# Performance work log

Measured on AMD Instinct MI355X. Metric: run time of the kernel, lower is better.

The kernel has to match this reference:

```python
import jax, jax.numpy as jnp
import numpy as np

B, D = 8192, 256
NUM_CLASSES = 128
CHUNK = 256          # matches module chunk_size; B % CHUNK == 0
TEMP = 0.07
EPS_NORM = 1e-12


def setup_inputs() -> dict:
    key = jax.random.key(0)
    k1, k2 = jax.random.split(key)
    features = jax.random.normal(k1, (B, D), dtype=jnp.float32)
    labels = jax.random.randint(k2, (B,), 0, NUM_CLASSES, dtype=jnp.int64)
    return {"features": features, "labels": labels}


def reference(features, labels):
    n = features.shape[0]
    temperature = max(TEMP, 1e-4)

    # F.normalize(dim=1): x / max(||x||, eps)
    norm = jnp.maximum(jnp.linalg.norm(features, axis=1, keepdims=True), EPS_NORM)
    f = features / norm
    # clamp is a no-op after normalization but kept for faithfulness
    f = jnp.clip(f, -1000.0, 1000.0)

    # [B, B] similarity; the torch loop computes exactly these rows chunk by chunk
    sim = jnp.matmul(f, f.T) / temperature

    # self-mask: each row i masks column i (diagonal of its chunk's square block)
    self_mask = ~jnp.eye(n, dtype=bool)

    # positive mask: same label, excluding self
    pos = (labels[:, None] == labels[None, :]) & self_mask
    # per-chunk fallback: if a 256-row chunk has no positives at all, use self_mask
    pos_c = pos.reshape(n // CHUNK, CHUNK, n)
    has_pos = pos_c.any(axis=(1, 2), keepdims=True)
    pos = jnp.where(has_pos, pos_c, self_mask.reshape(n // CHUNK, CHUNK, n)).reshape(n, n)

    # max-subtract BEFORE self-masking (faithful: includes self-sim = 1/temp)
    sim_max = jnp.max(sim, axis=1, keepdims=True)
    logits = jnp.clip(sim - jax.lax.stop_gradient(sim_max), -1000.0, 1000.0)

    exp_sim = jnp.maximum(jnp.exp(logits), 1e-8) * self_mask
    log_sum_exp = jnp.log(jnp.sum(exp_sim, axis=1, keepdims=True) + 1e-8)
    log_prob = jnp.maximum(logits - log_sum_exp, -1000.0)

    pos_pairs = jnp.sum(pos, axis=1)                      # [B] int
    row_loss = -jnp.sum(pos * log_prob, axis=1)           # [B]
    valid = pos_pairs > 0
    row_loss = jnp.where(valid, row_loss / jnp.maximum(pos_pairs, 1).astype(row_loss.dtype), 0.0)

    total_loss = jnp.sum(row_loss)
    total_pairs = jnp.sum(valid).astype(jnp.float32)
    mean_loss = total_loss / (total_pairs + 1e-8)
    loss = mean_loss  # reduction == 'mean'
    return loss, total_pairs, mean_loss
```

## Files before the change

kernel.cpp:

```cpp
#include <hip/hip_runtime.h>
#include <hip/hip_bf16.h>
#include <type_traits>

#define NB 8192
#define DD 256
#define INV_T (1.0f/0.07f)
#define LOG2E 1.4426950408889634f
#define K1    (INV_T*LOG2E)
#define CEXP  6.2087204553847255e-7f
#define NSTRIP 32
#define TILE 256
#define BN 64
#define NITER 4
#define BUFB (BN*DD*2)

typedef __attribute__((ext_vector_type(8))) short s8v;
typedef __attribute__((ext_vector_type(4))) float f4v;
typedef unsigned int u32;
typedef unsigned short u16;

#define OFF_FB   0
#define OFF_SE   (4*1024*1024)
#define OFF_SP   (OFF_SE + NSTRIP*NB*4)
#define OFF_CL   (OFF_SP + NSTRIP*NB*4)
#define OFF_CV   (OFF_CL + 256)
#define OFF_CNT  (OFF_CV + 256)

__global__ void k_norm(const float* __restrict__ feat,
                       __hip_bfloat16* __restrict__ fb, int* __restrict__ cnt) {
    if (blockIdx.x == 0 && threadIdx.x == 0) *cnt = 0;
    const int t = threadIdx.x;
    const int w = t >> 6, l = t & 63;
    const int row = blockIdx.x * 4 + w;
    const float4 v = ((const float4*)feat)[row * 64 + l];
    float s = v.x * v.x + v.y * v.y + v.z * v.z + v.w * v.w;
    #pragma unroll
    for (int d = 32; d; d >>= 1) s += __shfl_xor(s, d, 64);
    const float scale = 1.0f / fmaxf(sqrtf(s), 1e-12f);
    __hip_bfloat16 h0 = __float2bfloat16(v.x * scale);
    __hip_bfloat16 h1 = __float2bfloat16(v.y * scale);
    __hip_bfloat16 h2 = __float2bfloat16(v.z * scale);
    __hip_bfloat16 h3 = __float2bfloat16(v.w * scale);
    ushort4 o;
    o.x = *(u16*)&h0; o.y = *(u16*)&h1; o.z = *(u16*)&h2; o.w = *(u16*)&h3;
    ((ushort4*)fb)[row * 64 + l] = o;
}

__launch_bounds__(512)
__global__ void k_main(const __hip_bfloat16* __restrict__ fb,
                       const int* __restrict__ lab,
                       float* __restrict__ SE, float* __restrict__ SP) {
    __shared__ __align__(16) char ldsB[2 * BUFB];
    __shared__ int ldsLab[TILE];
    __shared__ float ldsColE[8][TILE];
    __shared__ float ldsColP[8][TILE];
    const int tid = threadIdx.x;
    const int w = tid >> 6;
    const int l = tid & 63;
    const int l15 = l & 15, lg = l >> 4;

    int cb = 0, rem = blockIdx.x;
    while (rem >= NSTRIP - cb) { rem -= NSTRIP - cb; cb++; }
    const int rb = cb + rem;
    const int row0 = rb * TILE, col0 = cb * TILE;
    const int wbase = row0 + w * 32;

    if (tid < TILE) ldsLab[tid] = lab[col0 + tid];

    s8v a[2][8];
    #pragma unroll
    for (int m = 0; m < 2; m++)
        #pragma unroll
        for (int kk = 0; kk < 8; kk++)
            a[m][kk] = *(const s8v*)(fb + (wbase + m * 16 + l15) * DD + kk * 32 + lg * 8);

    int labr[8];
    #pragma unroll
    for (int m = 0; m < 2; m++)
        #pragma unroll
        for (int r = 0; r < 4; r++)
            labr[m * 4 + r] = lab[wbase + m * 16 + lg * 4 + r];

    float sE[8], sPa[8], colE[4], colP[4];
    #pragma unroll
    for (int i = 0; i < 8; i++) { sE[i] = 0.f; sPa[i] = 0.f; }
    #pragma unroll
    for (int i = 0; i < 4; i++) { colE[i] = 0.f; colP[i] = 0.f; }

    s8v st[4];
    auto load_tile = [&](int ct) {
        const char* gsrc = (const char*)fb + (size_t)(col0 + ct * BN) * (DD * 2);
        #pragma unroll
        for (int i = 0; i < 4; i++)
            st[i] = *(const s8v*)(gsrc + tid * 16 + i * 8192);
    };
    auto write_tile = [&](int bufoff) {
        #pragma unroll
        for (int i = 0; i < 4; i++) {
            const int x = tid * 16 + i * 8192;
            const int br = x >> 9, inrow = x & 511;
            *(s8v*)(ldsB + bufoff + (br * 512 | (inrow ^ ((br & 7) << 4)))) = st[i];
        }
    };

    auto run = [&](auto diagC) {
        constexpr bool DIAG = decltype(diagC)::value;
        load_tile(0);
        write_tile(0);
        __syncthreads();
        for (int ct = 0; ct < NITER; ct++) {
            const int curoff = (ct & 1) * BUFB;
            if (ct + 1 < NITER) load_tile(ct + 1);

            int lc[4];
            #pragma unroll
            for (int n = 0; n < 4; n++)
                lc[n] = ldsLab[ct * BN + n * 16 + l15];

            f4v acc[2][4];
            #pragma unroll
            for (int m = 0; m < 2; m++)
                #pragma unroll
                for (int n = 0; n < 4; n++)
                    acc[m][n] = (f4v){0.f, 0.f, 0.f, 0.f};

            #pragma unroll
            for (int kk = 0; kk < 8; kk++) {
                s8v bfr[4];
                #pragma unroll
                for (int n = 0; n < 4; n++) {
                    const int br = n * 16 + l15;
                    const int ad = (br * 512 + kk * 64 + lg * 16) ^ ((br & 7) << 4);
                    bfr[n] = *(const s8v*)(ldsB + curoff + ad);
                }
                #pragma unroll
                for (int m = 0; m < 2; m++)
                    #pragma unroll
                    for (int n = 0; n < 4; n++)
                        acc[m][n] = __builtin_amdgcn_mfma_f32_16x16x32_bf16(a[m][kk], bfr[n], acc[m][n], 0, 0, 0);
            }

            #pragma unroll
            for (int n = 0; n < 4; n++) {
                #pragma unroll
                for (int m = 0; m < 2; m++)
                    #pragma unroll
                    for (int r = 0; r < 4; r++) {
                        const int idx = m * 4 + r;
                        const float v = acc[m][n][r];
                        float e = exp2f(v * K1);
                        bool pos = (lc[n] == labr[idx]);
                        if (DIAG) {
                            const int row = wbase + m * 16 + lg * 4 + r;
                            const int coln = col0 + ct * BN + n * 16 + l15;
                            const bool nself = (row != coln);
                            e = nself ? e : 0.f;
                            pos = pos && nself;
                        }
                        const float pv = pos ? v : 0.f;
                        sE[idx] += e;
                        sPa[idx] += pv;
                        if (!DIAG) { colE[n] += e; colP[n] += pv; }
                    }
            }

            if (!DIAG) {
                #pragma unroll
                for (int n = 0; n < 4; n++) {
                    colE[n] += __shfl_xor(colE[n], 16, 64);
                    colE[n] += __shfl_xor(colE[n], 32, 64);
                    colP[n] += __shfl_xor(colP[n], 16, 64);
                    colP[n] += __shfl_xor(colP[n], 32, 64);
                }
                if (l < 16) {
                    #pragma unroll
                    for (int n = 0; n < 4; n++) {
                        ldsColE[w][ct * BN + n * 16 + l15] = colE[n];
                        ldsColP[w][ct * BN + n * 16 + l15] = colP[n];
                    }
                }
                #pragma unroll
                for (int n = 0; n < 4; n++) { colE[n] = 0.f; colP[n] = 0.f; }
            }

            if (ct + 1 < NITER) write_tile(curoff ^ BUFB);
            __syncthreads();
        }
    };
    if (rb == cb) run(std::true_type{}); else run(std::false_type{});

    #pragma unroll
    for (int idx = 0; idx < 8; idx++) {
        #pragma unroll
        for (int d = 1; d < 16; d <<= 1) {
            sE[idx]  += __shfl_xor(sE[idx], d, 16);
            sPa[idx] += __shfl_xor(sPa[idx], d, 16);
        }
    }
    if (l15 == 0) {
        #pragma unroll
        for (int idx = 0; idx < 8; idx++) {
            const int row = wbase + (idx >> 2) * 16 + lg * 4 + (idx & 3);
            SE[cb * NB + row] = sE[idx];
            SP[cb * NB + row] = sPa[idx];
        }
    }

    if (rb != cb) {
        __syncthreads();
        const int c = tid & 255;
        if (tid < 256) {
            float s = 0.f;
            #pragma unroll
            for (int w2 = 0; w2 < 8; w2++) s += ldsColE[w2][c];
            SE[rb * NB + col0 + c] = s;
        } else {
            float s = 0.f;
            #pragma unroll
            for (int w2 = 0; w2 < 8; w2++) s += ldsColP[w2][c];
            SP[rb * NB + col0 + c] = s;
        }
    }
}

__global__ void k_rows(const int* __restrict__ lab,
                       const float* __restrict__ SE, const float* __restrict__ SP,
                       float* __restrict__ CL, float* __restrict__ CV,
                       int* __restrict__ cnt, float* __restrict__ out) {
    __shared__ int h[128];
    const int t = threadIdx.x;
    if (t < 128) h[t] = 0;
    __syncthreads();
    #pragma unroll
    for (int i = 0; i < 32; i++)
        atomicAdd(&h[lab[t + i * 256]], 1);
    __syncthreads();

    const int row = blockIdx.x * 256 + t;
    float se = 0.f, spa = 0.f;
    #pragma unroll
    for (int s = 0; s < NSTRIP; s++) {
        se  += SE[s * NB + row];
        spa += SP[s * NB + row];
    }
    const int n = h[lab[row]] - 1;
    const float lse = logf(se * CEXP + 1e-8f);
    const bool valid = n > 0;
    float loss = valid ? (lse - (spa - (float)n) * INV_T / (float)n) : 0.f;
    float vf = valid ? 1.f : 0.f;
    #pragma unroll
    for (int d = 32; d; d >>= 1) { loss += __shfl_xor(loss, d, 64); vf += __shfl_xor(vf, d, 64); }
    __shared__ float pl[4], pv[4];
    __shared__ int isLast;
    if ((t & 63) == 0) { pl[t >> 6] = loss; pv[t >> 6] = vf; }
    __syncthreads();
    if (t == 0) {
        CL[blockIdx.x] = pl[0] + pl[1] + pl[2] + pl[3];
        CV[blockIdx.x] = pv[0] + pv[1] + pv[2] + pv[3];
        __threadfence();
        isLast = (atomicAdd(cnt, 1) == 31);
    }
    __syncthreads();
    if (isLast) {
        __threadfence();
        float lsum = (t < 32) ? CL[t] : 0.f;
        float vsum = (t < 32) ? CV[t] : 0.f;
        #pragma unroll
        for (int d = 32; d; d >>= 1) { lsum += __shfl_xor(lsum, d, 64); vsum += __shfl_xor(vsum, d, 64); }
        if (t == 0) {
            const float mean = lsum / (vsum + 1e-8f);
            out[0] = mean;
            out[1] = vsum;
            out[2] = mean;
        }
    }
}

extern "C" void kernel_launch(void* const* d_in, const int* in_sizes, int n_in,
                              void* d_out, int out_size, void* d_ws, size_t ws_size,
                              hipStream_t stream) {
    (void)in_sizes; (void)n_in; (void)out_size; (void)ws_size;
    const float* feat = (const float*)d_in[0];
    const int*   lab  = (const int*)d_in[1];
    char* ws = (char*)d_ws;
    __hip_bfloat16* fb = (__hip_bfloat16*)(ws + OFF_FB);
    float* SE = (float*)(ws + OFF_SE);
    float* SP = (float*)(ws + OFF_SP);
    float* CL = (float*)(ws + OFF_CL);
    float* CV = (float*)(ws + OFF_CV);
    int*   cnt = (int*)(ws + OFF_CNT);
    float* out = (float*)d_out;

    hipLaunchKernelGGL(k_norm, dim3(NB / 4), dim3(256), 0, stream, feat, fb, cnt);
    hipLaunchKernelGGL(k_main, dim3(528), dim3(512), 0, stream, fb, lab, SE, SP);
    hipLaunchKernelGGL(k_rows, dim3(NB / 256), dim3(256), 0, stream, lab, SE, SP, CL, CV, cnt, out);
}
```

Baseline: 74.22 us.

## Shrink Gram tiles to 128 and stage column tiles via direct global-to-LDS loads

Halves the triangular tile size to 128 rows with 256-thread blocks, giving 2080 blocks instead of 528 so the work balances better across CUs and more blocks fit per CU. The register-staged tile loads are replaced with global_load_lds direct-to-LDS copies, with the XOR swizzle moved to the source address. Column partial sums are now folded into LDS accumulators every iteration, which adds an extra barrier per step. Smaller tiles reuse each loaded B tile less and double the number of strip partials, so the reduction in k_rows has more to sum.

```diff
diff --git a/kernel.cpp b/kernel.cpp
--- a/kernel.cpp
+++ b/kernel.cpp
@@ -8,11 +8,12 @@
 #define LOG2E 1.4426950408889634f
 #define K1    (INV_T*LOG2E)
 #define CEXP  6.2087204553847255e-7f
-#define NSTRIP 32
-#define TILE 256
-#define BN 64
+#define NSTRIP 64
+#define TILE 128
+#define BN 32
 #define NITER 4
 #define BUFB (BN*DD*2)
+#define NTILES (NSTRIP*(NSTRIP+1)/2)
 
 typedef __attribute__((ext_vector_type(8))) short s8v;
 typedef __attribute__((ext_vector_type(4))) float f4v;
@@ -46,14 +47,21 @@
     ((ushort4*)fb)[row * 64 + l] = o;
 }
 
-__launch_bounds__(512)
+__device__ __forceinline__ void gld16(const void* g, void* l) {
+    __builtin_amdgcn_global_load_lds((const __attribute__((address_space(1))) u32*)g,
+                                     (__attribute__((address_space(3))) u32*)l, 16, 0, 0);
+}
+
+__launch_bounds__(256, 4)
 __global__ void k_main(const __hip_bfloat16* __restrict__ fb,
                        const int* __restrict__ lab,
                        float* __restrict__ SE, float* __restrict__ SP) {
     __shared__ __align__(16) char ldsB[2 * BUFB];
     __shared__ int ldsLab[TILE];
-    __shared__ float ldsColE[8][TILE];
-    __shared__ float ldsColP[8][TILE];
+    __shared__ float ldsColE[4][BN];
+    __shared__ float ldsColP[4][BN];
+    __shared__ float colAccE[TILE];
+    __shared__ float colAccP[TILE];
     const int tid = threadIdx.x;
     const int w = tid >> 6;
     const int l = tid & 63;
@@ -65,7 +73,11 @@
     const int row0 = rb * TILE, col0 = cb * TILE;
     const int wbase = row0 + w * 32;
 
-    if (tid < TILE) ldsLab[tid] = lab[col0 + tid];
+    if (tid < TILE) {
+        ldsLab[tid] = lab[col0 + tid];
+        colAccE[tid] = 0.f;
+        colAccP[tid] = 0.f;
+    }
 
     s8v a[2][8];
     #pragma unroll
@@ -81,67 +93,55 @@
         for (int r = 0; r < 4; r++)
             labr[m * 4 + r] = lab[wbase + m * 16 + lg * 4 + r];
 
-    float sE[8], sPa[8], colE[4], colP[4];
+    float sE[8], sPa[8];
     #pragma unroll
     for (int i = 0; i < 8; i++) { sE[i] = 0.f; sPa[i] = 0.f; }
-    #pragma unroll
-    for (int i = 0; i < 4; i++) { colE[i] = 0.f; colP[i] = 0.f; }
-
-    s8v st[4];
-    auto load_tile = [&](int ct) {
-        const char* gsrc = (const char*)fb + (size_t)(col0 + ct * BN) * (DD * 2);
-        #pragma unroll
-        for (int i = 0; i < 4; i++)
-            st[i] = *(const s8v*)(gsrc + tid * 16 + i * 8192);
-    };
-    auto write_tile = [&](int bufoff) {
+
+    auto stage = [&](int ct, int bufoff) {
+        const char* gt = (const char*)fb + (size_t)(col0 + ct * BN) * (DD * 2);
         #pragma unroll
         for (int i = 0; i < 4; i++) {
-            const int x = tid * 16 + i * 8192;
-            const int br = x >> 9, inrow = x & 511;
-            *(s8v*)(ldsB + bufoff + (br * 512 | (inrow ^ ((br & 7) << 4)))) = st[i];
+            const int x = i * 4096 + (tid << 4);
+            const int br = x >> 9;
+            const int inrow = x & 511;
+            gld16(gt + br * 512 + (inrow ^ ((br & 7) << 4)),
+                  ldsB + bufoff + i * 4096 + w * 1024);
         }
     };
 
     auto run = [&](auto diagC) {
         constexpr bool DIAG = decltype(diagC)::value;
-        load_tile(0);
-        write_tile(0);
+        stage(0, 0);
         __syncthreads();
         for (int ct = 0; ct < NITER; ct++) {
             const int curoff = (ct & 1) * BUFB;
-            if (ct + 1 < NITER) load_tile(ct + 1);
-
-            int lc[4];
+            if (ct + 1 < NITER) stage(ct + 1, curoff ^ BUFB);
+
+            const int lc0 = ldsLab[ct * BN + l15];
+            const int lc1 = ldsLab[ct * BN + 16 + l15];
+
+            f4v acc[2][2];
             #pragma unroll
-            for (int n = 0; n < 4; n++)
-                lc[n] = ldsLab[ct * BN + n * 16 + l15];
-
-            f4v acc[2][4];
-            #pragma unroll
-            for (int m = 0; m < 2; m++)
-                #pragma unroll
-                for (int n = 0; n < 4; n++)
-                    acc[m][n] = (f4v){0.f, 0.f, 0.f, 0.f};
+            for (int m = 0; m < 2; m++) {
+                acc[m][0] = (f4v){0.f, 0.f, 0.f, 0.f};
+                acc[m][1] = (f4v){0.f, 0.f, 0.f, 0.f};
+            }
 
             #pragma unroll
             for (int kk = 0; kk < 8; kk++) {
-                s8v bfr[4];
-                #pragma unroll
-                for (int n = 0; n < 4; n++) {
-                    const int br = n * 16 + l15;
-                    const int ad = (br * 512 + kk * 64 + lg * 16) ^ ((br & 7) << 4);
-                    bfr[n] = *(const s8v*)(ldsB + curoff + ad);
-                }
-                #pragma unroll
-                for (int m = 0; m < 2; m++)
-                    #pragma unroll
-                    for (int n = 0; n < 4; n++)
-                        acc[m][n] = __builtin_amdgcn_mfma_f32_16x16x32_bf16(a[m][kk], bfr[n], acc[m][n], 0, 0, 0);
-            }
-
+                const int br0 = l15, br1 = 16 + l15;
+                s8v b0 = *(const s8v*)(ldsB + curoff + ((br0 * 512 + kk * 64 + lg * 16) ^ ((br0 & 7) << 4)));
+                s8v b1 = *(const s8v*)(ldsB + curoff + ((br1 * 512 + kk * 64 + lg * 16) ^ ((br1 & 7) << 4)));
+                acc[0][0] = __builtin_amdgcn_mfma_f32_16x16x32_bf16(a[0][kk], b0, acc[0][0], 0, 0, 0);
+                acc[1][0] = __builtin_amdgcn_mfma_f32_16x16x32_bf16(a[1][kk], b0, acc[1][0], 0, 0, 0);
+                acc[0][1] = __builtin_amdgcn_mfma_f32_16x16x32_bf16(a[0][kk], b1, acc[0][1], 0, 0, 0);
+                acc[1][1] = __builtin_amdgcn_mfma_f32_16x16x32_bf16(a[1][kk], b1, acc[1][1], 0, 0, 0);
+            }
+
+            float cE[2] = {0.f, 0.f}, cP[2] = {0.f, 0.f};
             #pragma unroll
-            for (int n = 0; n < 4; n++) {
+            for (int n = 0; n < 2; n++) {
+                const int lcn = n ? lc1 : lc0;
                 #pragma unroll
                 for (int m = 0; m < 2; m++)
                     #pragma unroll
@@ -149,7 +149,7 @@
                         const int idx = m * 4 + r;
                         const float v = acc[m][n][r];
                         float e = exp2f(v * K1);
-                        bool pos = (lc[n] == labr[idx]);
+                        bool pos = (lcn == labr[idx]);
                         if (DIAG) {
                             const int row = wbase + m * 16 + lg * 4 + r;
                             const int coln = col0 + ct * BN + n * 16 + l15;
@@ -160,31 +160,37 @@
                         const float pv = pos ? v : 0.f;
                         sE[idx] += e;
                         sPa[idx] += pv;
-                        if (!DIAG) { colE[n] += e; colP[n] += pv; }
+                        if (!DIAG) { cE[n] += e; cP[n] += pv; }
                     }
             }
 
             if (!DIAG) {
                 #pragma unroll
-                for (int n = 0; n < 4; n++) {
-                    colE[n] += __shfl_xor(colE[n], 16, 64);
-                    colE[n] += __shfl_xor(colE[n], 32, 64);
-                    colP[n] += __shfl_xor(colP[n], 16, 64);
-                    colP[n] += __shfl_xor(colP[n], 32, 64);
+                for (int n = 0; n < 2; n++) {
+                    cE[n] += __shfl_xor(cE[n], 16, 64);
+                    cE[n] += __shfl_xor(cE[n], 32, 64);
+                    cP[n] += __shfl_xor(cP[n], 16, 64);
+                    cP[n] += __shfl_xor(cP[n], 32, 64);
                 }
                 if (l < 16) {
-                    #pragma unroll
-                    for (int n = 0; n < 4; n++) {
-                        ldsColE[w][ct * BN + n * 16 + l15] = colE[n];
-                        ldsColP[w][ct * BN + n * 16 + l15] = colP[n];
-                    }
+                    ldsColE[w][l15]      = cE[0];
+                    ldsColE[w][16 + l15] = cE[1];
+                    ldsColP[w][l15]      = cP[0];
+                    ldsColP[w][16 + l15] = cP[1];
                 }
-                #pragma unroll
-                for (int n = 0; n < 4; n++) { colE[n] = 0.f; colP[n] = 0.f; }
-            }
-
-            if (ct + 1 < NITER) write_tile(curoff ^ BUFB);
+            }
             __syncthreads();
+            if (!DIAG) {
+                if (tid < BN) {
+                    colAccE[ct * BN + tid] += ldsColE[0][tid] + ldsColE[1][tid]
+                                            + ldsColE[2][tid] + ldsColE[3][tid];
+                } else if (tid < 2 * BN) {
+                    const int c = tid - BN;
+                    colAccP[ct * BN + c] += ldsColP[0][c] + ldsColP[1][c]
+                                          + ldsColP[2][c] + ldsColP[3][c];
+                }
+                __syncthreads();
+            }
         }
     };
     if (rb == cb) run(std::true_type{}); else run(std::false_type{});
@@ -207,19 +213,8 @@
     }
 
     if (rb != cb) {
-        __syncthreads();
-        const int c = tid & 255;
-        if (tid < 256) {
-            float s = 0.f;
-            #pragma unroll
-            for (int w2 = 0; w2 < 8; w2++) s += ldsColE[w2][c];
-            SE[rb * NB + col0 + c] = s;
-        } else {
-            float s = 0.f;
-            #pragma unroll
-            for (int w2 = 0; w2 < 8; w2++) s += ldsColP[w2][c];
-            SP[rb * NB + col0 + c] = s;
-        }
+        if (tid < TILE) SE[rb * NB + col0 + tid] = colAccE[tid];
+        else            SP[rb * NB + col0 + (tid - TILE)] = colAccP[tid - TILE];
     }
 }
 
@@ -292,6 +287,6 @@
     float* out = (float*)d_out;
 
     hipLaunchKernelGGL(k_norm, dim3(NB / 4), dim3(256), 0, stream, feat, fb, cnt);
-    hipLaunchKernelGGL(k_main, dim3(528), dim3(512), 0, stream, fb, lab, SE, SP);
+    hipLaunchKernelGGL(k_main, dim3(NTILES), dim3(256), 0, stream, fb, lab, SE, SP);
     hipLaunchKernelGGL(k_rows, dim3(NB / 256), dim3(256), 0, stream, lab, SE, SP, CL, CV, cnt, out);
 }
```

Result: slower. 186.9 us (+151.8%).

## Stage B tiles via global_load_lds and pack column partials as bf16 pairs

Applied to the files above, without the earlier changes.

Replaces the register-staged global-to-LDS copy of the column tile with direct global_load_lds instructions. The XOR swizzle now moves to the global source address, so data lands in LDS already permuted without passing through VGPRs. Column partial sums are packed as bf16 E/P pairs in one smaller LDS array, cutting LDS footprint and the final reduction work. The risks are lower accuracy in the column sums from bf16 packing, and a possible race because the async LDS write into the other buffer has no explicit vmcnt wait before the barrier.

```diff
diff --git a/kernel.cpp b/kernel.cpp
--- a/kernel.cpp
+++ b/kernel.cpp
@@ -13,6 +13,7 @@
 #define BN 64
 #define NITER 4
 #define BUFB (BN*DD*2)
+#define NTILES (NSTRIP*(NSTRIP+1)/2)
 
 typedef __attribute__((ext_vector_type(8))) short s8v;
 typedef __attribute__((ext_vector_type(4))) float f4v;
@@ -25,6 +26,17 @@
 #define OFF_CL   (OFF_SP + NSTRIP*NB*4)
 #define OFF_CV   (OFF_CL + 256)
 #define OFF_CNT  (OFF_CV + 256)
+
+__device__ __forceinline__ u32 packEP(float e, float p) {
+    __hip_bfloat16 be = __float2bfloat16(e), bp = __float2bfloat16(p);
+    return (u32)*(u16*)&be | ((u32)*(u16*)&bp << 16);
+}
+__device__ __forceinline__ float unpLo(u32 x) {
+    u16 h = (u16)x; __hip_bfloat16 b = *(__hip_bfloat16*)&h; return __bfloat162float(b);
+}
+__device__ __forceinline__ float unpHi(u32 x) {
+    u16 h = (u16)(x >> 16); __hip_bfloat16 b = *(__hip_bfloat16*)&h; return __bfloat162float(b);
+}
 
 __global__ void k_norm(const float* __restrict__ feat,
                        __hip_bfloat16* __restrict__ fb, int* __restrict__ cnt) {
@@ -46,14 +58,18 @@
     ((ushort4*)fb)[row * 64 + l] = o;
 }
 
+__device__ __forceinline__ void gld16(const void* g, void* l) {
+    __builtin_amdgcn_global_load_lds((const __attribute__((address_space(1))) u32*)g,
+                                     (__attribute__((address_space(3))) u32*)l, 16, 0, 0);
+}
+
 __launch_bounds__(512)
 __global__ void k_main(const __hip_bfloat16* __restrict__ fb,
                        const int* __restrict__ lab,
                        float* __restrict__ SE, float* __restrict__ SP) {
     __shared__ __align__(16) char ldsB[2 * BUFB];
     __shared__ int ldsLab[TILE];
-    __shared__ float ldsColE[8][TILE];
-    __shared__ float ldsColP[8][TILE];
+    __shared__ u32 ldsCol[8][NITER][BN];
     const int tid = threadIdx.x;
     const int w = tid >> 6;
     const int l = tid & 63;
@@ -81,36 +97,29 @@
         for (int r = 0; r < 4; r++)
             labr[m * 4 + r] = lab[wbase + m * 16 + lg * 4 + r];
 
-    float sE[8], sPa[8], colE[4], colP[4];
+    float sE[8], sPa[8];
     #pragma unroll
     for (int i = 0; i < 8; i++) { sE[i] = 0.f; sPa[i] = 0.f; }
-    #pragma unroll
-    for (int i = 0; i < 4; i++) { colE[i] = 0.f; colP[i] = 0.f; }
-
-    s8v st[4];
-    auto load_tile = [&](int ct) {
-        const char* gsrc = (const char*)fb + (size_t)(col0 + ct * BN) * (DD * 2);
-        #pragma unroll
-        for (int i = 0; i < 4; i++)
-            st[i] = *(const s8v*)(gsrc + tid * 16 + i * 8192);
-    };
-    auto write_tile = [&](int bufoff) {
+
+    auto stage = [&](int ct, int bufoff) {
+        const char* gt = (const char*)fb + (size_t)(col0 + ct * BN) * (DD * 2);
         #pragma unroll
         for (int i = 0; i < 4; i++) {
-            const int x = tid * 16 + i * 8192;
-            const int br = x >> 9, inrow = x & 511;
-            *(s8v*)(ldsB + bufoff + (br * 512 | (inrow ^ ((br & 7) << 4)))) = st[i];
+            const int x = i * 8192 + (tid << 4);
+            const int br = x >> 9;
+            const int inrow = x & 511;
+            gld16(gt + br * 512 + (inrow ^ ((br & 7) << 4)),
+                  ldsB + bufoff + i * 8192 + w * 1024);
         }
     };
 
     auto run = [&](auto diagC) {
         constexpr bool DIAG = decltype(diagC)::value;
-        load_tile(0);
-        write_tile(0);
+        stage(0, 0);
         __syncthreads();
         for (int ct = 0; ct < NITER; ct++) {
             const int curoff = (ct & 1) * BUFB;
-            if (ct + 1 < NITER) load_tile(ct + 1);
+            if (ct + 1 < NITER) stage(ct + 1, curoff ^ BUFB);
 
             int lc[4];
             #pragma unroll
@@ -140,6 +149,9 @@
                         acc[m][n] = __builtin_amdgcn_mfma_f32_16x16x32_bf16(a[m][kk], bfr[n], acc[m][n], 0, 0, 0);
             }
 
+            float cE[4], cP[4];
+            #pragma unroll
+            for (int n = 0; n < 4; n++) { cE[n] = 0.f; cP[n] = 0.f; }
             #pragma unroll
             for (int n = 0; n < 4; n++) {
                 #pragma unroll
@@ -160,30 +172,24 @@
                         const float pv = pos ? v : 0.f;
                         sE[idx] += e;
                         sPa[idx] += pv;
-                        if (!DIAG) { colE[n] += e; colP[n] += pv; }
+                        if (!DIAG) { cE[n] += e; cP[n] += pv; }
                     }
             }
 
             if (!DIAG) {
                 #pragma unroll
                 for (int n = 0; n < 4; n++) {
-                    colE[n] += __shfl_xor(colE[n], 16, 64);
-                    colE[n] += __shfl_xor(colE[n], 32, 64);
-                    colP[n] += __shfl_xor(colP[n], 16, 64);
-                    colP[n] += __shfl_xor(colP[n], 32, 64);
+                    cE[n] += __shfl_xor(cE[n], 16, 64);
+                    cE[n] += __shfl_xor(cE[n], 32, 64);
+                    cP[n] += __shfl_xor(cP[n], 16, 64);
+                    cP[n] += __shfl_xor(cP[n], 32, 64);
                 }
                 if (l < 16) {
                     #pragma unroll
-                    for (int n = 0; n < 4; n++) {
-                        ldsColE[w][ct * BN + n * 16 + l15] = colE[n];
-                        ldsColP[w][ct * BN + n * 16 + l15] = colP[n];
-                    }
+                    for (int n = 0; n < 4; n++)
+                        ldsCol[w][ct][n * 16 + l15] = packEP(cE[n], cP[n]);
                 }
-                #pragma unroll
-                for (int n = 0; n < 4; n++) { colE[n] = 0.f; colP[n] = 0.f; }
             }
-
-            if (ct + 1 < NITER) write_tile(curoff ^ BUFB);
             __syncthreads();
         }
     };
@@ -206,20 +212,17 @@
         }
     }
 
-    if (rb != cb) {
-        __syncthreads();
-        const int c = tid & 255;
-        if (tid < 256) {
-            float s = 0.f;
-            #pragma unroll
-            for (int w2 = 0; w2 < 8; w2++) s += ldsColE[w2][c];
-            SE[rb * NB + col0 + c] = s;
-        } else {
-            float s = 0.f;
-            #pragma unroll
-            for (int w2 = 0; w2 < 8; w2++) s += ldsColP[w2][c];
-            SP[rb * NB + col0 + c] = s;
-        }
+    if (rb != cb && tid < TILE) {
+        const int ct = tid >> 6, j = tid & 63;
+        float e = 0.f, p = 0.f;
+        #pragma unroll
+        for (int w2 = 0; w2 < 8; w2++) {
+            const u32 x = ldsCol[w2][ct][j];
+            e += unpLo(x);
+            p += unpHi(x);
+        }
+        SE[rb * NB + col0 + tid] = e;
+        SP[rb * NB + col0 + tid] = p;
     }
 }
 
@@ -292,6 +295,6 @@
     float* out = (float*)d_out;
 
     hipLaunchKernelGGL(k_norm, dim3(NB / 4), dim3(256), 0, stream, feat, fb, cnt);
-    hipLaunchKernelGGL(k_main, dim3(528), dim3(512), 0, stream, fb, lab, SE, SP);
+    hipLaunchKernelGGL(k_main, dim3(NTILES), dim3(512), 0, stream, fb, lab, SE, SP);
     hipLaunchKernelGGL(k_rows, dim3(NB / 256), dim3(256), 0, stream, lab, SE, SP, CL, CV, cnt, out);
 }
```

New measurement: 75.87 us. 1.02x slower.
